# Performance work log

Measured on AMD Instinct MI355X. Metric: run time of the kernel, lower is better.

Reference implementation:

```python
import jax, jax.numpy as jnp
import numpy as np

N, M, K, P = 200000, 50000, 32, 15
IN_DIM, OUT_DIM = 128, 256
HID = OUT_DIM // 4
KP_EXTENT = 0.05
KP_RADIUS = 0.06
EPS = 1e-5
SLOPE = 0.1


def _lrelu(x):
    return jnp.where(x > 0, x, SLOPE * x)


def _conv1d_bn_lrelu(x, W, b, g, beta):
    # pointwise conv (1x1) + batch-norm over points + leaky relu
    x = x @ W + b
    mu = jnp.mean(x, axis=0)
    var = jnp.var(x, axis=0)
    x = (x - mu) * jax.lax.rsqrt(var + EPS) * g + beta
    return _lrelu(x)


def _kpconv_pool(points, sub_points, pools, feats, kernel_points, kp_w):
    # KPConv with strided pooling: query = sub_points [M,3], support = points [N,3]
    nbr_pts = points[pools] - sub_points[:, None, :]              # [M,K,3] relative neighbor coords
    diff = nbr_pts[:, :, None, :] - kernel_points[None, None]     # [M,K,P,3]
    dist = jnp.sqrt(jnp.sum(diff * diff, axis=-1))                # [M,K,P]
    w = jnp.maximum(0.0, 1.0 - dist / KP_EXTENT)                  # linear correlation influence
    nbr_f = feats[pools]                                          # [M,K,C]
    agg = jnp.einsum('mkp,mkc->mpc', w, nbr_f)                    # per-kernel-point aggregation
    return jnp.einsum('mpc,pcd->md', agg, kp_w)                   # [M,C_out]


def setup_inputs() -> dict:
    key = jax.random.key(0)
    ks = jax.random.split(key, 10)
    points = jax.random.uniform(ks[0], (N, 3), dtype=jnp.float32) * 0.1
    sub_points = jax.random.uniform(ks[1], (M, 3), dtype=jnp.float32) * 0.1
    features = jax.random.normal(ks[2], (N, IN_DIM), dtype=jnp.float32)
    pools = jax.random.randint(ks[3], (M, K), 0, N, dtype=jnp.int32)
    kernel_points = jax.random.uniform(ks[4], (P, 3), minval=-KP_RADIUS, maxval=KP_RADIUS, dtype=jnp.float32)
    s_in = 1.0 / np.sqrt(IN_DIM)
    s_h = 1.0 / np.sqrt(HID)
    W1 = jax.random.normal(ks[5], (IN_DIM, HID), dtype=jnp.float32) * s_in
    kp_w = jax.random.normal(ks[6], (P, HID, HID), dtype=jnp.float32) * s_h
    W2 = jax.random.normal(ks[7], (HID, OUT_DIM), dtype=jnp.float32) * s_h
    Ws = jax.random.normal(ks[8], (IN_DIM, OUT_DIM), dtype=jnp.float32) * s_in
    return dict(
        points=points, sub_points=sub_points, features=features, pools=pools,
        kernel_points=kernel_points,
        W1=W1, b1=jnp.zeros((HID,)), g1=jnp.ones((HID,)), be1=jnp.zeros((HID,)),
        kp_w=kp_w,
        W2=W2, b2=jnp.zeros((OUT_DIM,)), g2=jnp.ones((OUT_DIM,)), be2=jnp.zeros((OUT_DIM,)),
        Ws=Ws, bs=jnp.zeros((OUT_DIM,)), gs=jnp.ones((OUT_DIM,)), bes=jnp.zeros((OUT_DIM,)),
    )


def reference(points, sub_points, features, pools, kernel_points,
              W1, b1, g1, be1, kp_w, W2, b2, g2, be2, Ws, bs, gs, bes):
    # main branch: Conv1D -> KPConvPools -> leaky_relu -> Conv1D
    x = _conv1d_bn_lrelu(features, W1, b1, g1, be1)               # [N,HID]
    x = _kpconv_pool(points, sub_points, pools, x, kernel_points, kp_w)  # [M,HID]
    x = _lrelu(x)
    x = _conv1d_bn_lrelu(x, W2, b2, g2, be2)                      # [M,OUT]
    # shortcut: MaxPoolNeighbors -> Conv1D
    sc = jnp.max(features[pools], axis=1)                         # [M,IN]
    sc = _conv1d_bn_lrelu(sc, Ws, bs, gs, bes)                    # [M,OUT]
    return _lrelu(x + sc)
```

## Files before the change

kernel.cpp:

```cpp
#include <hip/hip_runtime.h>

typedef unsigned short ushort_t;
typedef unsigned int uint_t;
typedef __attribute__((ext_vector_type(8))) short bf8_t;
typedef __attribute__((ext_vector_type(4))) float f4_t;
typedef __attribute__((ext_vector_type(4))) unsigned int u4_t;

#define NPTS 200000
#define MSUB 50000
#define KNBR 32
#define PK 15
#define INDIM 128
#define OUTDIM 256
#define HID 64
#define QD2 1024
#define NB1 1563
#define NBT 1563

__device__ __forceinline__ ushort_t f2bf(float f) {
  uint_t u = __float_as_uint(f);
  u = (u + 0x7fffu + ((u >> 16) & 1u)) >> 16;
  return (ushort_t)u;
}
__device__ __forceinline__ float bf2f(ushort_t h) {
  return __uint_as_float(((uint_t)h) << 16);
}
__device__ __forceinline__ float lrelu(float x) { return fmaxf(x, 0.1f * x); }
__device__ __forceinline__ f4_t zero4() { f4_t z = {0.f, 0.f, 0.f, 0.f}; return z; }

__global__ void prep_w_kernel(const float* __restrict__ W1, const float* __restrict__ W2,
                              const float* __restrict__ Ws, const float* __restrict__ kpw,
                              ushort_t* __restrict__ W1t, ushort_t* __restrict__ W2t,
                              ushort_t* __restrict__ Wst, ushort_t* __restrict__ kpwT2) {
  const int base = blockIdx.x * blockDim.x + threadIdx.x;
  const int stride = gridDim.x * blockDim.x;
  for (int t = base; t < HID * INDIM; t += stride) {
    int c = t & 63, k = t >> 6;
    W1t[c * INDIM + k] = f2bf(W1[k * HID + c]);
  }
  for (int t = base; t < OUTDIM * HID; t += stride) {
    int c = t & 255, k = t >> 8;
    W2t[c * HID + k] = f2bf(W2[k * OUTDIM + c]);
  }
  for (int t = base; t < OUTDIM * INDIM; t += stride) {
    int c = t & 255, k = t >> 8;
    Wst[c * INDIM + k] = f2bf(Ws[k * OUTDIM + c]);
  }
  for (int t = base; t < HID * QD2; t += stride) {
    int d = t >> 10, s = t & 1023;
    int nl = s & 1, r16v = (s >> 1) & 15, gv = (s >> 5) & 3, nh = (s >> 7) & 1, rr = (s >> 8) & 3;
    int p = gv * 4 + rr, c = r16v + (nh * 2 + nl) * 16;
    float v = (p < PK) ? kpw[((long)p * HID + c) * HID + d] : 0.f;
    kpwT2[d * QD2 + s] = f2bf(v);
  }
}

__global__ __launch_bounds__(256) void conv1_kernel(const float* __restrict__ feat,
                                                    const ushort_t* __restrict__ W1t,
                                                    ushort_t* __restrict__ feat16,
                                                    ushort_t* __restrict__ x1,
                                                    float* __restrict__ part1) {
  const int tid = threadIdx.x, wid = tid >> 6, lane = tid & 63;
  const int g = lane >> 4, r16 = lane & 15;
  const int rowbase = blockIdx.x * 128 + wid * 32;
  f4_t acc[2][4];
#pragma unroll
  for (int mi = 0; mi < 2; ++mi)
#pragma unroll
    for (int ni = 0; ni < 4; ++ni) acc[mi][ni] = zero4();
#pragma unroll
  for (int kc = 0; kc < 4; ++kc) {
    const int k0 = kc * 32 + g * 8;
    bf8_t a[2], b[4];
#pragma unroll
    for (int mi = 0; mi < 2; ++mi) {
      const int row = rowbase + mi * 16 + r16;
      const int rowc = (row < NPTS) ? row : 0;
      const float4 f0 = *(const float4*)(feat + (long)rowc * INDIM + k0);
      const float4 f1 = *(const float4*)(feat + (long)rowc * INDIM + k0 + 4);
      a[mi][0] = (short)f2bf(f0.x); a[mi][1] = (short)f2bf(f0.y);
      a[mi][2] = (short)f2bf(f0.z); a[mi][3] = (short)f2bf(f0.w);
      a[mi][4] = (short)f2bf(f1.x); a[mi][5] = (short)f2bf(f1.y);
      a[mi][6] = (short)f2bf(f1.z); a[mi][7] = (short)f2bf(f1.w);
      if (row < NPTS) *(bf8_t*)(feat16 + (long)row * INDIM + k0) = a[mi];
    }
#pragma unroll
    for (int ni = 0; ni < 4; ++ni)
      b[ni] = *(const bf8_t*)(W1t + (r16 + ni * 16) * INDIM + k0);
#pragma unroll
    for (int mi = 0; mi < 2; ++mi)
#pragma unroll
      for (int ni = 0; ni < 4; ++ni)
        acc[mi][ni] = __builtin_amdgcn_mfma_f32_16x16x32_bf16(a[mi], b[ni], acc[mi][ni], 0, 0, 0);
  }
  __shared__ float red[2][64];
  if (tid < 64) { red[0][tid] = 0.f; red[1][tid] = 0.f; }
  __syncthreads();
  float cs[4] = {0.f, 0.f, 0.f, 0.f}, cq[4] = {0.f, 0.f, 0.f, 0.f};
#pragma unroll
  for (int mi = 0; mi < 2; ++mi)
#pragma unroll
    for (int rr = 0; rr < 4; ++rr) {
      const int row = rowbase + mi * 16 + g * 4 + rr;
      if (row < NPTS) {
#pragma unroll
        for (int ni = 0; ni < 4; ++ni) {
          const float v = acc[mi][ni][rr];
          cs[ni] += v;
          cq[ni] += v * v;
          x1[(long)row * HID + r16 + ni * 16] = f2bf(v);
        }
      }
    }
#pragma unroll
  for (int ni = 0; ni < 4; ++ni) {
    atomicAdd(&red[0][r16 + ni * 16], cs[ni]);
    atomicAdd(&red[1][r16 + ni * 16], cq[ni]);
  }
  __syncthreads();
  if (tid < 128) {
    const float v = (tid < 64) ? red[0][tid] : red[1][tid - 64];
    part1[(long)tid * NB1 + blockIdx.x] = v;
  }
}

__global__ __launch_bounds__(256) void reduce1fin_kernel(const float* __restrict__ part1,
                                                         const float* __restrict__ g1,
                                                         const float* __restrict__ be1,
                                                         float* __restrict__ st) {
  const int c = blockIdx.x, tid = threadIdx.x;
  const int slot = (tid < 128) ? c : (64 + c);
  const float* src = part1 + (long)slot * NB1;
  float acc = 0.f;
  for (int i = tid & 127; i < NB1; i += 128) acc += src[i];
  __shared__ float sm[256];
  sm[tid] = acc;
  __syncthreads();
  for (int s = 64; s > 0; s >>= 1) {
    if ((tid & 127) < s) sm[tid] += sm[tid + s];
    __syncthreads();
  }
  if (tid == 0) {
    const float mu = sm[0] / (float)NPTS;
    const float var = sm[128] / (float)NPTS - mu * mu;
    const float a = g1[c] * rsqrtf(var + 1e-5f);
    st[c] = a;
    st[64 + c] = be1[c] - mu * a;
  }
}

__global__ __launch_bounds__(256) void gkp_kernel(
    const float* __restrict__ points, const float* __restrict__ subp,
    const int* __restrict__ pools, const float* __restrict__ kp,
    const ushort_t* __restrict__ x1, const ushort_t* __restrict__ feat16,
    const float* __restrict__ st, const ushort_t* __restrict__ kpwT2,
    ushort_t* __restrict__ x2, ushort_t* __restrict__ scmax) {
  const int tid = threadIdx.x, wid = tid >> 6, lane = tid & 63;
  const int g = lane >> 4, r16 = lane & 15, l31 = lane & 31;
  const int mbase = blockIdx.x * 16;
  __shared__ __align__(16) char aggT[16 * 2048];
  __shared__ __align__(16) uint_t ft2[4][32][36];
  __shared__ float pts[4][32][3];
  __shared__ int idxs[4][32];
  float A4[4], S4[4];
#pragma unroll
  for (int ni = 0; ni < 4; ++ni) {
    A4[ni] = st[r16 + ni * 16];
    S4[ni] = st[64 + r16 + ni * 16];
  }
  const int p = r16;
  const int pc = (p < PK) ? p : 0;
  const float kx = kp[pc * 3 + 0], ky = kp[pc * 3 + 1], kz = kp[pc * 3 + 2];

  for (int mm = 0; mm < 4; ++mm) {
    const int m = mbase + wid * 4 + mm;
    const int lm = wid * 4 + mm;
    if (lane < 32) idxs[wid][lane] = pools[m * KNBR + lane];
    if (lane < 32) {
      const int n = idxs[wid][lane];
      pts[wid][lane][0] = points[n * 3 + 0];
      pts[wid][lane][1] = points[n * 3 + 1];
      pts[wid][lane][2] = points[n * 3 + 2];
    }
#pragma unroll
    for (int i = 0; i < 16; ++i) {
      const int k = 2 * i + (lane >> 5);
      const int n = idxs[wid][k];
      ft2[wid][l31][k] = *(const uint_t*)(x1 + (long)n * HID + l31 * 2);
    }
    const float sx = subp[m * 3 + 0], sy = subp[m * 3 + 1], sz = subp[m * 3 + 2];
    bf8_t afrag;
#pragma unroll
    for (int j = 0; j < 8; ++j) {
      const int k = g * 8 + j;
      const float dx = pts[wid][k][0] - sx - kx;
      const float dy = pts[wid][k][1] - sy - ky;
      const float dz = pts[wid][k][2] - sz - kz;
      const float dist = sqrtf(dx * dx + dy * dy + dz * dz);
      float w = fmaxf(0.f, 1.f - dist * 20.f);
      if (p >= PK) w = 0.f;
      afrag[j] = (short)f2bf(w);
    }
    f4_t acc[4];
#pragma unroll
    for (int ni = 0; ni < 4; ++ni) acc[ni] = zero4();
#pragma unroll
    for (int ni = 0; ni < 4; ++ni) {
      const int c = r16 + ni * 16;
      const int c2 = c >> 1;
      const int sh = (c & 1) * 16;
      const float A = A4[ni], S = S4[ni];
      const uint_t* src = &ft2[wid][c2][g * 8];
      const u4_t v0 = *(const u4_t*)src;
      const u4_t v1 = *(const u4_t*)(src + 4);
      bf8_t bfrag;
#pragma unroll
      for (int j = 0; j < 4; ++j) {
        const float xa = __uint_as_float(((v0[j] >> sh) & 0xffffu) << 16);
        bfrag[j] = (short)f2bf(lrelu(A * xa + S));
        const float xb = __uint_as_float(((v1[j] >> sh) & 0xffffu) << 16);
        bfrag[4 + j] = (short)f2bf(lrelu(A * xb + S));
      }
      acc[ni] = __builtin_amdgcn_mfma_f32_16x16x32_bf16(afrag, bfrag, acc[ni], 0, 0, 0);
    }
    char* rowp = aggT + lm * 2048;
#pragma unroll
    for (int rr = 0; rr < 4; ++rr)
#pragma unroll
      for (int nh = 0; nh < 2; ++nh) {
        const uint_t v =
            (uint_t)f2bf(acc[nh * 2][rr]) | ((uint_t)f2bf(acc[nh * 2 + 1][rr]) << 16);
        int byte = ((rr * 2 + nh) * 64 + g * 16 + r16) * 4;
        byte ^= (lm & 7) << 4;
        *(uint_t*)(rowp + byte) = v;
      }
    float mx0 = -3.0e38f, mx1 = -3.0e38f;
#pragma unroll
    for (int k = 0; k < KNBR; ++k) {
      const int n = idxs[wid][k];
      const uint_t v = *(const uint_t*)(feat16 + (long)n * INDIM + lane * 2);
      mx0 = fmaxf(mx0, __uint_as_float(v << 16));
      mx1 = fmaxf(mx1, __uint_as_float(v & 0xffff0000u));
    }
    ((uint_t*)scmax)[(long)m * 64 + lane] =
        (uint_t)(__float_as_uint(mx0) >> 16) | (__float_as_uint(mx1) & 0xffff0000u);
  }
  __syncthreads();
  f4_t acc2 = zero4();
  const ushort_t* brow = kpwT2 + (long)(wid * 16 + r16) * QD2;
#pragma unroll 8
  for (int kc = 0; kc < 32; ++kc) {
    int byte = (kc * 64 + g * 16) ^ ((r16 & 7) << 4);
    const bf8_t a = *(const bf8_t*)(aggT + r16 * 2048 + byte);
    const bf8_t b = *(const bf8_t*)(brow + kc * 32 + g * 8);
    acc2 = __builtin_amdgcn_mfma_f32_16x16x32_bf16(a, b, acc2, 0, 0, 0);
  }
#pragma unroll
  for (int rr = 0; rr < 4; ++rr) {
    const int m = mbase + g * 4 + rr;
    x2[(long)m * HID + wid * 16 + r16] = f2bf(lrelu(acc2[rr]));
  }
}

template <int KD>
__device__ __forceinline__ void convT_body(const ushort_t* __restrict__ A,
                                           const ushort_t* __restrict__ Bt,
                                           ushort_t* __restrict__ Oraw,
                                           float* __restrict__ part, int blk) {
  const int tid = threadIdx.x, lane = tid & 63;
  const int wid = tid >> 6;
  const int g = lane >> 4, r16 = lane & 15;
  const int rowbase = blk * 32;
  const int colbase = wid * 64;
  f4_t acc[2][4];
#pragma unroll
  for (int mi = 0; mi < 2; ++mi)
#pragma unroll
    for (int ni = 0; ni < 4; ++ni) acc[mi][ni] = zero4();
#pragma unroll
  for (int kc = 0; kc < KD / 32; ++kc) {
    const int k0 = kc * 32 + g * 8;
    bf8_t a[2], b[4];
#pragma unroll
    for (int mi = 0; mi < 2; ++mi) {
      int row = rowbase + mi * 16 + r16;
      if (row >= MSUB) row = 0;
      a[mi] = *(const bf8_t*)(A + (long)row * KD + k0);
    }
#pragma unroll
    for (int ni = 0; ni < 4; ++ni)
      b[ni] = *(const bf8_t*)(Bt + (long)(colbase + r16 + ni * 16) * KD + k0);
#pragma unroll
    for (int mi = 0; mi < 2; ++mi)
#pragma unroll
      for (int ni = 0; ni < 4; ++ni)
        acc[mi][ni] = __builtin_amdgcn_mfma_f32_16x16x32_bf16(a[mi], b[ni], acc[mi][ni], 0, 0, 0);
  }
  __shared__ float red[2][256];
  red[0][tid] = 0.f;
  red[1][tid] = 0.f;
  __syncthreads();
  float cs[4] = {0.f, 0.f, 0.f, 0.f}, cq[4] = {0.f, 0.f, 0.f, 0.f};
#pragma unroll
  for (int mi = 0; mi < 2; ++mi)
#pragma unroll
    for (int rr = 0; rr < 4; ++rr) {
      const int row = rowbase + mi * 16 + g * 4 + rr;
      if (row < MSUB) {
#pragma unroll
        for (int ni = 0; ni < 4; ++ni) {
          const float v = acc[mi][ni][rr];
          cs[ni] += v;
          cq[ni] += v * v;
          Oraw[(long)row * OUTDIM + colbase + r16 + ni * 16] = f2bf(v);
        }
      }
    }
#pragma unroll
  for (int ni = 0; ni < 4; ++ni) {
    atomicAdd(&red[0][colbase + r16 + ni * 16], cs[ni]);
    atomicAdd(&red[1][colbase + r16 + ni * 16], cq[ni]);
  }
  __syncthreads();
  part[(long)tid * NBT + blk] = red[0][tid];
  part[(long)(256 + tid) * NBT + blk] = red[1][tid];
}

__global__ __launch_bounds__(256) void convT_merged_kernel(
    const ushort_t* __restrict__ x2, const ushort_t* __restrict__ W2t,
    const ushort_t* __restrict__ scmax, const ushort_t* __restrict__ Wst,
    ushort_t* __restrict__ x3, ushort_t* __restrict__ scraw,
    float* __restrict__ part2, float* __restrict__ part3) {
  const int b = blockIdx.x;
  if (b < NBT)
    convT_body<HID>(x2, W2t, x3, part2, b);
  else
    convT_body<INDIM>(scmax, Wst, scraw, part3, b - NBT);
}

__global__ __launch_bounds__(256) void reduce23fin_kernel(const float* __restrict__ part2,
                                                          const float* __restrict__ part3,
                                                          const float* __restrict__ g2,
                                                          const float* __restrict__ be2,
                                                          const float* __restrict__ gs,
                                                          const float* __restrict__ bes,
                                                          float* __restrict__ st) {
  const int blk = blockIdx.x, tid = threadIdx.x;
  const int sc = blk >> 8, c = blk & 255;
  const float* part = sc ? part3 : part2;
  const int slot = (tid < 128) ? c : (256 + c);
  const float* src = part + (long)slot * NBT;
  float acc = 0.f;
  for (int i = tid & 127; i < NBT; i += 128) acc += src[i];
  __shared__ float sm[256];
  sm[tid] = acc;
  __syncthreads();
  for (int s = 64; s > 0; s >>= 1) {
    if ((tid & 127) < s) sm[tid] += sm[tid + s];
    __syncthreads();
  }
  if (tid == 0) {
    const float mu = sm[0] / (float)MSUB;
    const float var = sm[128] / (float)MSUB - mu * mu;
    const float a = (sc ? gs : g2)[c] * rsqrtf(var + 1e-5f);
    const int off = sc ? 640 : 128;
    st[off + c] = a;
    st[off + 256 + c] = (sc ? bes : be2)[c] - mu * a;
  }
}

__global__ __launch_bounds__(256) void final_kernel(const ushort_t* __restrict__ x3,
                                                    const ushort_t* __restrict__ sc,
                                                    const float* __restrict__ st,
                                                    float* __restrict__ out) {
  const int i = blockIdx.x * 256 + threadIdx.x;
  const int c0 = (i * 4) & 255;
  const uint2 xv = ((const uint2*)x3)[i];
  const uint2 sv = ((const uint2*)sc)[i];
  float xs[4] = {bf2f((ushort_t)(xv.x & 0xffffu)), bf2f((ushort_t)(xv.x >> 16)),
                 bf2f((ushort_t)(xv.y & 0xffffu)), bf2f((ushort_t)(xv.y >> 16))};
  float ss[4] = {bf2f((ushort_t)(sv.x & 0xffffu)), bf2f((ushort_t)(sv.x >> 16)),
                 bf2f((ushort_t)(sv.y & 0xffffu)), bf2f((ushort_t)(sv.y >> 16))};
  float r[4];
#pragma unroll
  for (int j = 0; j < 4; ++j) {
    const int c = c0 + j;
    const float v = lrelu(st[128 + c] * xs[j] + st[384 + c]);
    const float u = lrelu(st[640 + c] * ss[j] + st[896 + c]);
    r[j] = lrelu(v + u);
  }
  ((float4*)out)[i] = make_float4(r[0], r[1], r[2], r[3]);
}

extern "C" void kernel_launch(void* const* d_in, const int* in_sizes, int n_in,
                              void* d_out, int out_size, void* d_ws, size_t ws_size,
                              hipStream_t stream) {
  (void)in_sizes; (void)n_in; (void)out_size;
  const float* points = (const float*)d_in[0];
  const float* subp = (const float*)d_in[1];
  const float* feat = (const float*)d_in[2];
  const int* pools = (const int*)d_in[3];
  const float* kp = (const float*)d_in[4];
  const float* W1 = (const float*)d_in[5];
  const float* g1 = (const float*)d_in[7];
  const float* be1 = (const float*)d_in[8];
  const float* kpw = (const float*)d_in[9];
  const float* W2 = (const float*)d_in[10];
  const float* g2 = (const float*)d_in[12];
  const float* be2 = (const float*)d_in[13];
  const float* Wsm = (const float*)d_in[14];
  const float* gs = (const float*)d_in[16];
  const float* bes = (const float*)d_in[17];
  float* out = (float*)d_out;

  char* w = (char*)d_ws;
  size_t o = 0;
  ushort_t* feat16 = (ushort_t*)(w + o); o += (size_t)NPTS * INDIM * 2;
  ushort_t* x1 = (ushort_t*)(w + o);     o += (size_t)NPTS * HID * 2;
  ushort_t* x2 = (ushort_t*)(w + o);     o += (size_t)MSUB * HID * 2;
  ushort_t* x3 = (ushort_t*)(w + o);     o += (size_t)MSUB * OUTDIM * 2;
  ushort_t* scmax = (ushort_t*)(w + o);  o += (size_t)MSUB * INDIM * 2;
  ushort_t* scraw = (ushort_t*)(w + o);  o += (size_t)MSUB * OUTDIM * 2;
  float* part1 = (float*)(w + o);        o += (size_t)128 * NB1 * 4;
  float* part2 = (float*)(w + o);        o += (size_t)512 * NBT * 4;
  float* part3 = (float*)(w + o);        o += (size_t)512 * NBT * 4;
  ushort_t* W1t = (ushort_t*)(w + o);    o += HID * INDIM * 2;
  ushort_t* W2t = (ushort_t*)(w + o);    o += OUTDIM * HID * 2;
  ushort_t* Wst = (ushort_t*)(w + o);    o += OUTDIM * INDIM * 2;
  ushort_t* kpwT2 = (ushort_t*)(w + o);  o += HID * QD2 * 2;
  float* st = (float*)(w + o);           o += 1152 * 4;
  if (ws_size < o) return;

  prep_w_kernel<<<64, 256, 0, stream>>>(W1, W2, Wsm, kpw, W1t, W2t, Wst, kpwT2);
  conv1_kernel<<<NB1, 256, 0, stream>>>(feat, W1t, feat16, x1, part1);
  reduce1fin_kernel<<<64, 256, 0, stream>>>(part1, g1, be1, st);
  gkp_kernel<<<MSUB / 16, 256, 0, stream>>>(points, subp, pools, kp, x1, feat16, st,
                                            kpwT2, x2, scmax);
  convT_merged_kernel<<<2 * NBT, 256, 0, stream>>>(x2, W2t, scmax, Wst, x3, scraw,
                                                   part2, part3);
  reduce23fin_kernel<<<512, 256, 0, stream>>>(part2, part3, g2, be2, gs, bes, st);
  final_kernel<<<MSUB * OUTDIM / 1024, 256, 0, stream>>>(x3, scraw, st, out);
}
```

Before: 282.4 us.

## Double gkp block to 8 waves and replace LDS index/point staging with shuffles

The gather-KPConv kernel now launches 512 threads per block, with 8 waves each handling 2 sub-points instead of 4 waves handling 4. This raises the memory-level parallelism available for the random gathers. Neighbor indices and coordinates now stay in registers and are broadcast with __shfl instead of being staged in shared memory, and the subpoint/kernel-point offset is folded into one subtraction. Only the first 4 waves run the final kp_w MFMA stage, so half the block idles there. The ft2 shared buffer doubles in size, which may limit occupancy.

```diff
diff --git a/kernel.cpp b/kernel.cpp
--- a/kernel.cpp
+++ b/kernel.cpp
@@ -149,19 +149,17 @@
   }
 }
 
-__global__ __launch_bounds__(256) void gkp_kernel(
+__global__ __launch_bounds__(512, 4) void gkp_kernel(
     const float* __restrict__ points, const float* __restrict__ subp,
     const int* __restrict__ pools, const float* __restrict__ kp,
     const ushort_t* __restrict__ x1, const ushort_t* __restrict__ feat16,
     const float* __restrict__ st, const ushort_t* __restrict__ kpwT2,
     ushort_t* __restrict__ x2, ushort_t* __restrict__ scmax) {
   const int tid = threadIdx.x, wid = tid >> 6, lane = tid & 63;
-  const int g = lane >> 4, r16 = lane & 15, l31 = lane & 31;
+  const int g = lane >> 4, r16 = lane & 15, l31 = lane & 31, hi = lane >> 5;
   const int mbase = blockIdx.x * 16;
   __shared__ __align__(16) char aggT[16 * 2048];
-  __shared__ __align__(16) uint_t ft2[4][32][36];
-  __shared__ float pts[4][32][3];
-  __shared__ int idxs[4][32];
+  __shared__ __align__(16) uint_t ft2[8][32][36];
   float A4[4], S4[4];
 #pragma unroll
   for (int ni = 0; ni < 4; ++ni) {
@@ -172,30 +170,32 @@
   const int pc = (p < PK) ? p : 0;
   const float kx = kp[pc * 3 + 0], ky = kp[pc * 3 + 1], kz = kp[pc * 3 + 2];
 
-  for (int mm = 0; mm < 4; ++mm) {
-    const int m = mbase + wid * 4 + mm;
-    const int lm = wid * 4 + mm;
-    if (lane < 32) idxs[wid][lane] = pools[m * KNBR + lane];
+#pragma unroll
+  for (int mm = 0; mm < 2; ++mm) {
+    const int lm = wid * 2 + mm;
+    const int m = mbase + lm;
+    const int idx0 = pools[m * KNBR + l31];
+    float px = 0.f, py = 0.f, pz = 0.f;
     if (lane < 32) {
-      const int n = idxs[wid][lane];
-      pts[wid][lane][0] = points[n * 3 + 0];
-      pts[wid][lane][1] = points[n * 3 + 1];
-      pts[wid][lane][2] = points[n * 3 + 2];
+      px = points[idx0 * 3 + 0];
+      py = points[idx0 * 3 + 1];
+      pz = points[idx0 * 3 + 2];
     }
 #pragma unroll
     for (int i = 0; i < 16; ++i) {
-      const int k = 2 * i + (lane >> 5);
-      const int n = idxs[wid][k];
+      const int k = 2 * i + hi;
+      const int n = __shfl(idx0, k);
       ft2[wid][l31][k] = *(const uint_t*)(x1 + (long)n * HID + l31 * 2);
     }
     const float sx = subp[m * 3 + 0], sy = subp[m * 3 + 1], sz = subp[m * 3 + 2];
+    const float kxx = kx + sx, kyy = ky + sy, kzz = kz + sz;
     bf8_t afrag;
 #pragma unroll
     for (int j = 0; j < 8; ++j) {
       const int k = g * 8 + j;
-      const float dx = pts[wid][k][0] - sx - kx;
-      const float dy = pts[wid][k][1] - sy - ky;
-      const float dz = pts[wid][k][2] - sz - kz;
+      const float dx = __shfl(px, k) - kxx;
+      const float dy = __shfl(py, k) - kyy;
+      const float dz = __shfl(pz, k) - kzz;
       const float dist = sqrtf(dx * dx + dy * dy + dz * dz);
       float w = fmaxf(0.f, 1.f - dist * 20.f);
       if (p >= PK) w = 0.f;
@@ -237,7 +237,7 @@
     float mx0 = -3.0e38f, mx1 = -3.0e38f;
 #pragma unroll
     for (int k = 0; k < KNBR; ++k) {
-      const int n = idxs[wid][k];
+      const int n = __shfl(idx0, k);
       const uint_t v = *(const uint_t*)(feat16 + (long)n * INDIM + lane * 2);
       mx0 = fmaxf(mx0, __uint_as_float(v << 16));
       mx1 = fmaxf(mx1, __uint_as_float(v & 0xffff0000u));
@@ -246,19 +246,21 @@
         (uint_t)(__float_as_uint(mx0) >> 16) | (__float_as_uint(mx1) & 0xffff0000u);
   }
   __syncthreads();
-  f4_t acc2 = zero4();
-  const ushort_t* brow = kpwT2 + (long)(wid * 16 + r16) * QD2;
+  if (wid < 4) {
+    f4_t acc2 = zero4();
+    const ushort_t* brow = kpwT2 + (long)(wid * 16 + r16) * QD2;
 #pragma unroll 8
-  for (int kc = 0; kc < 32; ++kc) {
-    int byte = (kc * 64 + g * 16) ^ ((r16 & 7) << 4);
-    const bf8_t a = *(const bf8_t*)(aggT + r16 * 2048 + byte);
-    const bf8_t b = *(const bf8_t*)(brow + kc * 32 + g * 8);
-    acc2 = __builtin_amdgcn_mfma_f32_16x16x32_bf16(a, b, acc2, 0, 0, 0);
-  }
-#pragma unroll
-  for (int rr = 0; rr < 4; ++rr) {
-    const int m = mbase + g * 4 + rr;
-    x2[(long)m * HID + wid * 16 + r16] = f2bf(lrelu(acc2[rr]));
+    for (int kc = 0; kc < 32; ++kc) {
+      int byte = (kc * 64 + g * 16) ^ ((r16 & 7) << 4);
+      const bf8_t a = *(const bf8_t*)(aggT + r16 * 2048 + byte);
+      const bf8_t b = *(const bf8_t*)(brow + kc * 32 + g * 8);
+      acc2 = __builtin_amdgcn_mfma_f32_16x16x32_bf16(a, b, acc2, 0, 0, 0);
+    }
+#pragma unroll
+    for (int rr = 0; rr < 4; ++rr) {
+      const int m = mbase + g * 4 + rr;
+      x2[(long)m * HID + wid * 16 + r16] = f2bf(lrelu(acc2[rr]));
+    }
   }
 }
 
@@ -434,7 +436,7 @@
   prep_w_kernel<<<64, 256, 0, stream>>>(W1, W2, Wsm, kpw, W1t, W2t, Wst, kpwT2);
   conv1_kernel<<<NB1, 256, 0, stream>>>(feat, W1t, feat16, x1, part1);
   reduce1fin_kernel<<<64, 256, 0, stream>>>(part1, g1, be1, st);
-  gkp_kernel<<<MSUB / 16, 256, 0, stream>>>(points, subp, pools, kp, x1, feat16, st,
+  gkp_kernel<<<MSUB / 16, 512, 0, stream>>>(points, subp, pools, kp, x1, feat16, st,
                                             kpwT2, x2, scmax);
   convT_merged_kernel<<<2 * NBT, 256, 0, stream>>>(x2, W2t, scmax, Wst, x3, scraw,
                                                    part2, part3);
```

New measurement: 272.4 us. 1.04x faster.
